# Performance work log

Hardware: AMD Instinct MI355X
Metric: run time of the kernel (lower is better)

The kernel has to match this reference:

```python
import jax, jax.numpy as jnp
import numpy as np

B, QL, KL, D, H = 2, 512, 8192, 1024, 8
HD = D // H  # head dim = 128


def setup_inputs() -> dict:
    key = jax.random.key(0)
    ks = jax.random.split(key, 12)
    s = 0.02
    return {
        "inputs_q": jax.random.normal(ks[0], (B, QL, D), jnp.float32),
        "inputs_k": jax.random.normal(ks[1], (B, KL, D), jnp.float32),
        "inputs_v": jax.random.normal(ks[2], (B, KL, D), jnp.float32),
        "attention_mask": jax.random.randint(ks[3], (B, QL, KL), 0, 2).astype(bool),
        "Wq": jax.random.normal(ks[4], (D, D), jnp.float32) * s,
        "bq": jnp.zeros((D,), jnp.float32),
        "Wk": jax.random.normal(ks[5], (D, D), jnp.float32) * s,
        "bk": jnp.zeros((D,), jnp.float32),
        "Wv": jax.random.normal(ks[6], (D, D), jnp.float32) * s,
        "bv": jnp.zeros((D,), jnp.float32),
        "Wf": jax.random.normal(ks[7], (D, D), jnp.float32) * s,
        "bf": jnp.zeros((D,), jnp.float32),
    }


def reference(inputs_q, inputs_k, inputs_v, attention_mask, Wq, bq, Wk, bk, Wv, bv, Wf, bf):
    # Projections (torch Linear: x @ W.T + b)
    q = inputs_q @ Wq.T + bq  # [B, QL, D]
    k = inputs_k @ Wk.T + bk  # [B, KL, D]
    v = inputs_v @ Wv.T + bv  # [B, KL, D]

    q = q.reshape(B, QL, H, HD)
    k = k.reshape(B, KL, H, HD)
    v = v.reshape(B, KL, H, HD)

    # scores [B, H, QL, KL]
    scores = jnp.einsum("bqhd,bkhd->bhqk", q, k)
    scale = 1.0 / np.sqrt(HD).astype(np.float32)
    scores = scores * scale
    large_k = jnp.float32(1e30)
    scores = jnp.where(attention_mask[:, None, :, :], scores, -large_k)

    probs = jax.nn.softmax(scores, axis=-1)
    # note: original calls self.dropout(normalized) but discards the result -> no-op

    summed = jnp.einsum("bhqk,bkhd->bqhd", probs, v).reshape(B, QL, H * HD)

    # wipe rows whose mask is all zero
    wipe = jnp.all(~attention_mask, axis=2, keepdims=True)  # [B, QL, 1]
    summed = jnp.where(wipe, jnp.zeros_like(summed), summed)

    return summed @ Wf.T + bf
```

## Files before the change

### kernel.cpp

```cpp
#include <hip/hip_runtime.h>
#include <hip/hip_bf16.h>
#include <math.h>

typedef __attribute__((ext_vector_type(4))) float fx4;
typedef __attribute__((ext_vector_type(4))) short sx4;
typedef __attribute__((ext_vector_type(8))) short sx8;
typedef unsigned long long u64;

#define MFMA16(a, b, c) __builtin_amdgcn_mfma_f32_16x16x16bf16_1k(a, b, c, 0, 0, 0)
#define MFMA32(a, b, c) __builtin_amdgcn_mfma_f32_16x16x32_bf16(a, b, c, 0, 0, 0)

__device__ __forceinline__ unsigned short f2bf(float f) {
  unsigned int u = __float_as_uint(f);
  return (unsigned short)((u + 0x7fffu + ((u >> 16) & 1u)) >> 16);
}

typedef const __attribute__((address_space(1))) char* gc1p;
typedef __attribute__((address_space(3))) char* lc3p;
__device__ __forceinline__ void glds16(const void* g, const void* lds_uniform) {
  gc1p gp = (gc1p)(unsigned long long)(uintptr_t)g;
  lc3p lp = (lc3p)(unsigned)__builtin_amdgcn_readfirstlane((int)(unsigned)(uintptr_t)lds_uniform);
  __builtin_amdgcn_global_load_lds(gp, lp, 16, 0, 0);
}

__global__ __launch_bounds__(256) void k_prep(
    const float* __restrict__ ink, const float* __restrict__ inv,
    const float* __restrict__ inq, const float* __restrict__ Wq,
    const float* __restrict__ Wk, const float* __restrict__ Wv,
    const float* __restrict__ Wf, const int* __restrict__ mask, short* ck,
    short* cv, short* cq, short* cwq, short* cwk, short* cwv, short* cwf,
    u64* __restrict__ mb) {
  __shared__ unsigned char nib[256];
  const int bx = blockIdx.x;
  const int t = threadIdx.x;
  if (bx >= 18944) {
    const int mbx = bx - 18944;
    const int4 m = *(const int4*)(mask + (size_t)mbx * 1024 + t * 4);
    nib[t] = (unsigned char)((m.x != 0) | ((m.y != 0) << 1) | ((m.z != 0) << 2) |
                             ((m.w != 0) << 3));
    __syncthreads();
    if (t < 16) {
      u64 wv = 0;
#pragma unroll
      for (int i = 0; i < 16; i++) wv |= (u64)(nib[t * 16 + i] & 0xF) << (4 * i);
      mb[(size_t)mbx * 16 + t] = wv;
    }
    return;
  }
  const float* s;
  short* d;
  size_t i;
  if (bx < 8192) {
    s = ink; d = ck; i = (size_t)bx * 2048;
  } else if (bx < 16384) {
    s = inv; d = cv; i = (size_t)(bx - 8192) * 2048;
  } else if (bx < 16896) {
    s = inq; d = cq; i = (size_t)(bx - 16384) * 2048;
  } else {
    const int r = bx - 16896;
    const int seg = r >> 9;
    s = seg == 0 ? Wq : seg == 1 ? Wk : seg == 2 ? Wv : Wf;
    d = seg == 0 ? cwq : seg == 1 ? cwk : seg == 2 ? cwv : cwf;
    i = (size_t)(r & 511) * 2048;
  }
  i += (size_t)t * 8;
  const fx4 a = *(const fx4*)(s + i);
  const fx4 b = *(const fx4*)(s + i + 4);
  sx8 o;
  o[0] = (short)f2bf(a[0]); o[1] = (short)f2bf(a[1]);
  o[2] = (short)f2bf(a[2]); o[3] = (short)f2bf(a[3]);
  o[4] = (short)f2bf(b[0]); o[5] = (short)f2bf(b[1]);
  o[6] = (short)f2bf(b[2]); o[7] = (short)f2bf(b[3]);
  *(sx8*)(d + i) = o;
}

template <int MODE, int MT>
__device__ __forceinline__ void gemm_body(short* sA, short* sB,
                                          const short* __restrict__ A,
                                          const short* __restrict__ Bw,
                                          const float* __restrict__ bias,
                                          void* __restrict__ Cptr, int M, int N,
                                          int K, float alpha, int bx) {
  const int t = threadIdx.x;
  const int lane = t & 63;
  const int w = t >> 6;
  const int quad = lane >> 4;
  const int l16 = lane & 15;
  const int x7 = l16 & 7;
  int m0, n0;
  if (M >= 8192) {
    const int ml = bx & 7, nn = (bx >> 3) & 7, mh = bx >> 6;
    m0 = (mh * 8 + ml) * MT;
    n0 = nn << 7;
  } else {
    const int ntile = N >> 7;
    n0 = (bx % ntile) << 7;
    m0 = (bx / ntile) * MT;
  }
  constexpr int NI = (MT == 128) ? 4 : 2;
  const int wm = (MT == 128) ? ((w >> 1) << 6) : 0;
  const int wn = (MT == 128) ? ((w & 1) << 6) : (w << 5);
  const fx4 fzero = {0.f, 0.f, 0.f, 0.f};
  fx4 acc[4][NI];
#pragma unroll
  for (int i = 0; i < 4; i++)
#pragma unroll
    for (int j = 0; j < NI; j++) acc[i][j] = fzero;

  const int srow = lane >> 3;
  const int scb = lane & 7;

  for (int k0 = 0; k0 < K; k0 += 64) {
    __syncthreads();
    if (MT == 128) {
#pragma unroll
      for (int j = 0; j < 4; j++) {
        const int row = w * 32 + j * 8 + srow;
        const int cb = scb ^ (row & 7);
        glds16(A + (size_t)(m0 + row) * K + k0 + cb * 8, &sA[(w * 32 + j * 8) * 64]);
      }
    } else {
#pragma unroll
      for (int j = 0; j < 2; j++) {
        const int row = j * 32 + w * 8 + srow;
        const int cb = scb ^ (row & 7);
        glds16(A + (size_t)(m0 + row) * K + k0 + cb * 8, &sA[(j * 32 + w * 8) * 64]);
      }
    }
#pragma unroll
    for (int j = 0; j < 4; j++) {
      const int row = w * 32 + j * 8 + srow;
      const int cb = scb ^ (row & 7);
      glds16(Bw + (size_t)(n0 + row) * K + k0 + cb * 8, &sB[(w * 32 + j * 8) * 64]);
    }
    __syncthreads();
#pragma unroll
    for (int kc = 0; kc < 2; kc++) {
      const int cbp = ((kc * 4 + quad) ^ x7) * 8;
      sx8 fa[4], fb[NI];
#pragma unroll
      for (int i = 0; i < 4; i++)
        fa[i] = *(const sx8*)(&sA[(wm + i * 16 + l16) * 64 + cbp]);
#pragma unroll
      for (int i = 0; i < NI; i++)
        fb[i] = *(const sx8*)(&sB[(wn + i * 16 + l16) * 64 + cbp]);
#pragma unroll
      for (int mi = 0; mi < 4; mi++)
#pragma unroll
        for (int ni = 0; ni < NI; ni++)
          acc[mi][ni] = MFMA32(fa[mi], fb[ni], acc[mi][ni]);
    }
  }
#pragma unroll
  for (int ni = 0; ni < NI; ni++) {
    const int col = n0 + wn + ni * 16 + l16;
    const float bval = bias[col];
    if (MODE == 2) {
#pragma unroll
      for (int mi = 0; mi < 4; mi++) {
        const int rowb = m0 + wm + mi * 16 + quad * 4;
        const int bb = rowb >> 13;
        const int kl = (rowb & 8191) ^ ((col & 8) ? 4 : 0);
        sx4 pkv;
#pragma unroll
        for (int r = 0; r < 4; r++) pkv[r] = (short)f2bf(acc[mi][ni][r] + bval);
        *(sx4*)((unsigned short*)Cptr + ((size_t)bb * 1024 + col) * 8192 + kl) = pkv;
      }
    } else {
#pragma unroll
      for (int mi = 0; mi < 4; mi++)
#pragma unroll
        for (int r = 0; r < 4; r++) {
          const int row = m0 + wm + mi * 16 + quad * 4 + r;
          const float v = (acc[mi][ni][r] + bval) * alpha;
          if (MODE == 1) ((float*)Cptr)[(size_t)row * N + col] = v;
          else ((unsigned short*)Cptr)[(size_t)row * N + col] = f2bf(v);
        }
    }
  }
}

__global__ __launch_bounds__(256) void k_gemm_k(const short* __restrict__ ck,
                                                const short* __restrict__ cwk,
                                                const float* __restrict__ bk,
                                                short* __restrict__ Kp) {
  __shared__ __align__(16) short smem[16384];
  gemm_body<0, 128>(smem, smem + 8192, ck, cwk, bk, Kp, 16384, 1024, 1024, 1.f,
                    blockIdx.x);
}

__global__ __launch_bounds__(256) void k_proj_vq(
    const short* __restrict__ cv, const short* __restrict__ cwv,
    const float* __restrict__ bv, short* __restrict__ Vt,
    const short* __restrict__ cq, const short* __restrict__ cwq,
    const float* __restrict__ bq, short* __restrict__ Qp, float alpha_q) {
  __shared__ __align__(16) short smem[16384];
  const int bx = blockIdx.x;
  if (bx < 128)
    gemm_body<0, 64>(smem, smem + 8192, cq, cwq, bq, Qp, 1024, 1024, 1024,
                     alpha_q, bx);
  else
    gemm_body<2, 128>(smem, smem + 8192, cv, cwv, bv, Vt, 16384, 1024, 1024,
                      1.f, bx - 128);
}

__global__ __launch_bounds__(256) void k_gemm_out(const short* __restrict__ summed,
                                                  const short* __restrict__ cwf,
                                                  const float* __restrict__ bf,
                                                  float* __restrict__ out) {
  __shared__ __align__(16) short smem[16384];
  gemm_body<1, 64>(smem, smem + 8192, summed, cwf, bf, out, 1024, 1024, 1024,
                   1.f, blockIdx.x);
}

__global__ __launch_bounds__(256, 4) void k_attn(const short* __restrict__ Qp,
                                                 const short* __restrict__ Kp,
                                                 const short* __restrict__ Vt,
                                                 const u64* __restrict__ mb,
                                                 float* __restrict__ ml,
                                                 float* __restrict__ Op) {
  __shared__ __align__(16) short sK[8192];
  __shared__ __align__(16) short sV[8192];
  const int x = blockIdx.x;
  const int gl = x & 7;
  const int qt = (x >> 3) & 7;
  const int gh = x >> 6;
  const int g = gh * 8 + gl;
  const int s = g & 7;
  const int h = (g >> 3) & 7;
  const int b = g >> 6;
  const int li = ((b * 8 + h) * 8 + qt) * 8 + s;
  const int t = threadIdx.x;
  const int lane = t & 63;
  const int w = t >> 6;
  const int quad = lane >> 4;
  const int l16 = lane & 15;
  const int x7 = l16 & 7;
  const int q0 = qt << 6;
  const fx4 fzero = {0.f, 0.f, 0.f, 0.f};

  const short* qbase = Qp + (size_t)(b * 512 + q0 + w * 16 + l16) * 1024 + h * 128;
  sx8 aq[4];
#pragma unroll
  for (int kc = 0; kc < 4; kc++) aq[kc] = *(const sx8*)(qbase + kc * 32 + quad * 8);

  fx4 Ot[8];
#pragma unroll
  for (int d = 0; d < 8; d++) Ot[d] = fzero;
  float lsum = 0.f;

  const short* kbase = Kp + (size_t)(b * 8192 + s * 1024) * 1024 + h * 128;
  const short* vbase = Vt + (size_t)(b * 1024 + h * 128) * 8192 + s * 1024;
  const u64* wdp = mb + (size_t)(b * 512 + q0 + w * 16 + l16) * 128 + s * 16;
  const int srow4 = lane >> 4, scb16 = lane & 15;
  const int srow8 = lane >> 3, scb8 = lane & 7;
  const int h4 = ((quad & 1) ^ ((l16 >> 3) & 1)) * 4;

  for (int kt = 0; kt < 16; kt++) {
    __syncthreads();
#pragma unroll
    for (int j = 0; j < 4; j++) {
      const int row = (w * 4 + j) * 4 + srow4;
      const int cb = scb16 ^ (row & 7);
      glds16(kbase + (size_t)(kt * 64 + row) * 1024 + cb * 8, &sK[(w * 4 + j) * 512]);
    }
#pragma unroll
    for (int j = 0; j < 4; j++) {
      const int row = (w * 4 + j) * 8 + srow8;
      const int cb = scb8 ^ (row & 7);
      glds16(vbase + (size_t)row * 8192 + kt * 64 + cb * 8, &sV[(w * 4 + j) * 512]);
    }
    const u64 wd = wdp[kt];
    __syncthreads();
    const unsigned lo = (unsigned)wd, hi = (unsigned)(wd >> 32);
    sx4 pk[4];
#pragma unroll
    for (int nt = 0; nt < 4; nt++) {
      fx4 a = fzero;
#pragma unroll
      for (int kc = 0; kc < 4; kc++) {
        const sx8 kf = *(const sx8*)(&sK[(nt * 16 + l16) * 128 + ((kc * 4 + quad) ^ x7) * 8]);
        a = MFMA32(kf, aq[kc], a);
      }
      const unsigned bits = (nt & 2) ? hi : lo;
      const int sh = (nt & 1) * 16 + quad * 4;
      float pv[4];
#pragma unroll
      for (int r = 0; r < 4; r++) {
        const float e = __builtin_amdgcn_exp2f(a[r]);
        pv[r] = ((bits >> (sh + r)) & 1u) ? e : 0.f;
        lsum += pv[r];
      }
      sx4 pko;
      ((unsigned*)&pko)[0] = __builtin_amdgcn_perm(
          __float_as_uint(pv[1]) + 0x8000u, __float_as_uint(pv[0]) + 0x8000u, 0x07060302u);
      ((unsigned*)&pko)[1] = __builtin_amdgcn_perm(
          __float_as_uint(pv[3]) + 0x8000u, __float_as_uint(pv[2]) + 0x8000u, 0x07060302u);
      pk[nt] = pko;
    }
#pragma unroll
    for (int dt = 0; dt < 8; dt++) {
      fx4 o = Ot[dt];
#pragma unroll
      for (int nt = 0; nt < 4; nt++) {
        const int cb = (2 * nt + (quad >> 1)) ^ x7;
        const sx4 vf = *(const sx4*)(&sV[(dt * 16 + l16) * 64 + cb * 8 + h4]);
        o = MFMA16(vf, pk[nt], o);
      }
      Ot[dt] = o;
    }
  }
  lsum += __shfl_xor(lsum, 16, 64);
  lsum += __shfl_xor(lsum, 32, 64);
  if (lane < 16) ml[(size_t)li * 64 + w * 16 + l16] = lsum;
  float* ob = Op + (size_t)li * 8192 + (w * 16 + l16) * 128 + quad * 4;
#pragma unroll
  for (int dt = 0; dt < 8; dt++) *(fx4*)(ob + dt * 16) = Ot[dt];
}

__global__ __launch_bounds__(256) void k_combine(const float* __restrict__ ml,
                                                 const float* __restrict__ Op,
                                                 short* __restrict__ summed) {
  const int xc = blockIdx.x;
  const int qt = xc & 7;
  const int h = (xc >> 3) & 7;
  const int b = xc >> 6;
  const int t = threadIdx.x;
  const int row = t >> 2;
  const int dg = (t & 3) * 32;
  float L = 0.f;
#pragma unroll
  for (int s = 0; s < 8; s++) L += ml[(size_t)(xc * 8 + s) * 64 + row];
  float o[32];
#pragma unroll
  for (int i = 0; i < 32; i++) o[i] = 0.f;
  if (L != 0.f) {
#pragma unroll
    for (int s = 0; s < 8; s++) {
      const float* src = Op + (size_t)(xc * 8 + s) * 8192 + row * 128 + dg;
#pragma unroll
      for (int i = 0; i < 8; i++) {
        const fx4 v = *(const fx4*)(src + i * 4);
        o[i * 4 + 0] += v[0]; o[i * 4 + 1] += v[1];
        o[i * 4 + 2] += v[2]; o[i * 4 + 3] += v[3];
      }
    }
    const float inv = 1.f / L;
#pragma unroll
    for (int i = 0; i < 32; i++) o[i] *= inv;
  }
  short* dst = summed + (size_t)(b * 512 + qt * 64 + row) * 1024 + h * 128 + dg;
#pragma unroll
  for (int i = 0; i < 4; i++) {
    sx8 pkv;
#pragma unroll
    for (int j = 0; j < 8; j++) pkv[j] = (short)f2bf(o[i * 8 + j]);
    *(sx8*)(dst + i * 8) = pkv;
  }
}

extern "C" void kernel_launch(void* const* d_in, const int* in_sizes, int n_in,
                              void* d_out, int out_size, void* d_ws, size_t ws_size,
                              hipStream_t stream) {
  (void)in_sizes; (void)n_in; (void)out_size; (void)ws_size;
  const float* inq = (const float*)d_in[0];
  const float* ink = (const float*)d_in[1];
  const float* inv = (const float*)d_in[2];
  const int* mask = (const int*)d_in[3];
  const float* Wq = (const float*)d_in[4];
  const float* bq = (const float*)d_in[5];
  const float* Wk = (const float*)d_in[6];
  const float* bk = (const float*)d_in[7];
  const float* Wv = (const float*)d_in[8];
  const float* bv = (const float*)d_in[9];
  const float* Wf = (const float*)d_in[10];
  const float* bf = (const float*)d_in[11];

  char* ws = (char*)d_ws;
  short* S1 = (short*)(ws + 0);
  short* Kp = (short*)(ws + 33554432);
  short* S3 = (short*)(ws + 67108864);
  short* cq = (short*)(ws + 100663296);
  short* cwq = (short*)(ws + 102760448);
  short* cwk = (short*)(ws + 104857600);
  short* cwv = (short*)(ws + 106954752);
  short* cwf = (short*)(ws + 109051904);
  short* Qp = (short*)(ws + 111149056);
  short* summed = (short*)(ws + 113246208);
  u64* mb = (u64*)(ws + 115343360);
  float* ml = (float*)(ws + 116391936);

  const float alpha_q = 0.12751757f;

  k_prep<<<27136, 256, 0, stream>>>(ink, inv, inq, Wq, Wk, Wv, Wf, mask, S1, S3,
                                    cq, cwq, cwk, cwv, cwf, mb);
  k_gemm_k<<<1024, 256, 0, stream>>>(S1, cwk, bk, Kp);
  k_proj_vq<<<1152, 256, 0, stream>>>(S3, cwv, bv, S1, cq, cwq, bq, Qp, alpha_q);
  k_attn<<<1024, 256, 0, stream>>>(Qp, Kp, S1, mb, ml, (float*)S3);
  k_combine<<<128, 256, 0, stream>>>(ml, (const float*)S3, summed);
  k_gemm_out<<<128, 256, 0, stream>>>(summed, cwf, bf, (float*)d_out);
}
```

Baseline: 388.7 us.

## Fuse fp32-to-bf16 activation conversion into projection GEMM tile loads

Removes the separate conversion pass over the Q, K and V activations in the prep kernel. The projection GEMMs now read fp32 inputs directly into registers, pack them to bf16 with v_cvt_pk_bf16_f32, and store them into the swizzled LDS tile. This drops a full write and re-read of the large bf16 copies of K and V. In exchange, the A operand no longer uses async global-to-LDS loads, so global load latency is exposed before each tile sync and register pressure rises.

```diff
diff --git a/kernel.cpp b/kernel.cpp
--- a/kernel.cpp
+++ b/kernel.cpp
@@ -13,6 +13,12 @@
 __device__ __forceinline__ unsigned short f2bf(float f) {
   unsigned int u = __float_as_uint(f);
   return (unsigned short)((u + 0x7fffu + ((u >> 16) & 1u)) >> 16);
+}
+
+__device__ __forceinline__ unsigned cvtpk(float lo, float hi) {
+  unsigned r;
+  asm("v_cvt_pk_bf16_f32 %0, %1, %2" : "=v"(r) : "v"(lo), "v"(hi));
+  return r;
 }
 
 typedef const __attribute__((address_space(1))) char* gc1p;
@@ -24,17 +30,15 @@
 }
 
 __global__ __launch_bounds__(256) void k_prep(
-    const float* __restrict__ ink, const float* __restrict__ inv,
-    const float* __restrict__ inq, const float* __restrict__ Wq,
-    const float* __restrict__ Wk, const float* __restrict__ Wv,
-    const float* __restrict__ Wf, const int* __restrict__ mask, short* ck,
-    short* cv, short* cq, short* cwq, short* cwk, short* cwv, short* cwf,
-    u64* __restrict__ mb) {
+    const float* __restrict__ Wq, const float* __restrict__ Wk,
+    const float* __restrict__ Wv, const float* __restrict__ Wf,
+    const int* __restrict__ mask, short* cwq, short* cwk, short* cwv,
+    short* cwf, u64* __restrict__ mb) {
   __shared__ unsigned char nib[256];
   const int bx = blockIdx.x;
   const int t = threadIdx.x;
-  if (bx >= 18944) {
-    const int mbx = bx - 18944;
+  if (bx >= 2048) {
+    const int mbx = bx - 2048;
     const int4 m = *(const int4*)(mask + (size_t)mbx * 1024 + t * 4);
     nib[t] = (unsigned char)((m.x != 0) | ((m.y != 0) << 1) | ((m.z != 0) << 2) |
                              ((m.w != 0) << 3));
@@ -47,23 +51,10 @@
     }
     return;
   }
-  const float* s;
-  short* d;
-  size_t i;
-  if (bx < 8192) {
-    s = ink; d = ck; i = (size_t)bx * 2048;
-  } else if (bx < 16384) {
-    s = inv; d = cv; i = (size_t)(bx - 8192) * 2048;
-  } else if (bx < 16896) {
-    s = inq; d = cq; i = (size_t)(bx - 16384) * 2048;
-  } else {
-    const int r = bx - 16896;
-    const int seg = r >> 9;
-    s = seg == 0 ? Wq : seg == 1 ? Wk : seg == 2 ? Wv : Wf;
-    d = seg == 0 ? cwq : seg == 1 ? cwk : seg == 2 ? cwv : cwf;
-    i = (size_t)(r & 511) * 2048;
-  }
-  i += (size_t)t * 8;
+  const int seg = bx >> 9;
+  const float* s = seg == 0 ? Wq : seg == 1 ? Wk : seg == 2 ? Wv : Wf;
+  short* d = seg == 0 ? cwq : seg == 1 ? cwk : seg == 2 ? cwv : cwf;
+  size_t i = (size_t)(bx & 511) * 2048 + (size_t)t * 8;
   const fx4 a = *(const fx4*)(s + i);
   const fx4 b = *(const fx4*)(s + i + 4);
   sx8 o;
@@ -74,9 +65,9 @@
   *(sx8*)(d + i) = o;
 }
 
-template <int MODE, int MT>
+template <int MODE, int MT, int AF32>
 __device__ __forceinline__ void gemm_body(short* sA, short* sB,
-                                          const short* __restrict__ A,
+                                          const void* __restrict__ Aptr,
                                           const short* __restrict__ Bw,
                                           const float* __restrict__ bias,
                                           void* __restrict__ Cptr, int M, int N,
@@ -98,6 +89,7 @@
     m0 = (bx / ntile) * MT;
   }
   constexpr int NI = (MT == 128) ? 4 : 2;
+  constexpr int NJ = (MT == 128) ? 4 : 2;
   const int wm = (MT == 128) ? ((w >> 1) << 6) : 0;
   const int wn = (MT == 128) ? ((w & 1) << 6) : (w << 5);
   const fx4 fzero = {0.f, 0.f, 0.f, 0.f};
@@ -111,20 +103,28 @@
   const int scb = lane & 7;
 
   for (int k0 = 0; k0 < K; k0 += 64) {
+    fx4 ra[NJ][2];
+    if (AF32) {
+      const float* Af = (const float*)Aptr;
+#pragma unroll
+      for (int j = 0; j < NJ; j++) {
+        const int rbase = (MT == 128) ? (w * 32 + j * 8) : (j * 32 + w * 8);
+        const int row = rbase + srow;
+        const int cb = scb ^ (row & 7);
+        const float* src = Af + (size_t)(m0 + row) * K + k0 + cb * 8;
+        ra[j][0] = *(const fx4*)src;
+        ra[j][1] = *(const fx4*)(src + 4);
+      }
+    }
     __syncthreads();
-    if (MT == 128) {
-#pragma unroll
-      for (int j = 0; j < 4; j++) {
-        const int row = w * 32 + j * 8 + srow;
+    if (!AF32) {
+      const short* A = (const short*)Aptr;
+#pragma unroll
+      for (int j = 0; j < NJ; j++) {
+        const int rbase = (MT == 128) ? (w * 32 + j * 8) : (j * 32 + w * 8);
+        const int row = rbase + srow;
         const int cb = scb ^ (row & 7);
-        glds16(A + (size_t)(m0 + row) * K + k0 + cb * 8, &sA[(w * 32 + j * 8) * 64]);
-      }
-    } else {
-#pragma unroll
-      for (int j = 0; j < 2; j++) {
-        const int row = j * 32 + w * 8 + srow;
-        const int cb = scb ^ (row & 7);
-        glds16(A + (size_t)(m0 + row) * K + k0 + cb * 8, &sA[(j * 32 + w * 8) * 64]);
+        glds16(A + (size_t)(m0 + row) * K + k0 + cb * 8, &sA[rbase * 64]);
       }
     }
 #pragma unroll
@@ -132,6 +132,19 @@
       const int row = w * 32 + j * 8 + srow;
       const int cb = scb ^ (row & 7);
       glds16(Bw + (size_t)(n0 + row) * K + k0 + cb * 8, &sB[(w * 32 + j * 8) * 64]);
+    }
+    if (AF32) {
+#pragma unroll
+      for (int j = 0; j < NJ; j++) {
+        const int rbase = (MT == 128) ? (w * 32 + j * 8) : (j * 32 + w * 8);
+        sx8 o;
+        unsigned* ou = (unsigned*)&o;
+        ou[0] = cvtpk(ra[j][0][0], ra[j][0][1]);
+        ou[1] = cvtpk(ra[j][0][2], ra[j][0][3]);
+        ou[2] = cvtpk(ra[j][1][0], ra[j][1][1]);
+        ou[3] = cvtpk(ra[j][1][2], ra[j][1][3]);
+        *(sx8*)(&sA[rbase * 64 + lane * 8]) = o;
+      }
     }
     __syncthreads();
 #pragma unroll
@@ -180,28 +193,28 @@
   }
 }
 
-__global__ __launch_bounds__(256) void k_gemm_k(const short* __restrict__ ck,
+__global__ __launch_bounds__(256) void k_gemm_k(const float* __restrict__ ink,
                                                 const short* __restrict__ cwk,
                                                 const float* __restrict__ bk,
                                                 short* __restrict__ Kp) {
   __shared__ __align__(16) short smem[16384];
-  gemm_body<0, 128>(smem, smem + 8192, ck, cwk, bk, Kp, 16384, 1024, 1024, 1.f,
-                    blockIdx.x);
+  gemm_body<0, 128, 1>(smem, smem + 8192, ink, cwk, bk, Kp, 16384, 1024, 1024,
+                       1.f, blockIdx.x);
 }
 
 __global__ __launch_bounds__(256) void k_proj_vq(
-    const short* __restrict__ cv, const short* __restrict__ cwv,
+    const float* __restrict__ inv, const short* __restrict__ cwv,
     const float* __restrict__ bv, short* __restrict__ Vt,
-    const short* __restrict__ cq, const short* __restrict__ cwq,
+    const float* __restrict__ inq, const short* __restrict__ cwq,
     const float* __restrict__ bq, short* __restrict__ Qp, float alpha_q) {
   __shared__ __align__(16) short smem[16384];
   const int bx = blockIdx.x;
   if (bx < 128)
-    gemm_body<0, 64>(smem, smem + 8192, cq, cwq, bq, Qp, 1024, 1024, 1024,
-                     alpha_q, bx);
+    gemm_body<0, 64, 1>(smem, smem + 8192, inq, cwq, bq, Qp, 1024, 1024, 1024,
+                        alpha_q, bx);
   else
-    gemm_body<2, 128>(smem, smem + 8192, cv, cwv, bv, Vt, 16384, 1024, 1024,
-                      1.f, bx - 128);
+    gemm_body<2, 128, 1>(smem, smem + 8192, inv, cwv, bv, Vt, 16384, 1024, 1024,
+                         1.f, bx - 128);
 }
 
 __global__ __launch_bounds__(256) void k_gemm_out(const short* __restrict__ summed,
@@ -209,8 +222,8 @@
                                                   const float* __restrict__ bf,
                                                   float* __restrict__ out) {
   __shared__ __align__(16) short smem[16384];
-  gemm_body<1, 64>(smem, smem + 8192, summed, cwf, bf, out, 1024, 1024, 1024,
-                   1.f, blockIdx.x);
+  gemm_body<1, 64, 0>(smem, smem + 8192, summed, cwf, bf, out, 1024, 1024, 1024,
+                      1.f, blockIdx.x);
 }
 
 __global__ __launch_bounds__(256, 4) void k_attn(const short* __restrict__ Qp,
@@ -377,10 +390,9 @@
   const float* bf = (const float*)d_in[11];
 
   char* ws = (char*)d_ws;
-  short* S1 = (short*)(ws + 0);
+  short* Vt = (short*)(ws + 0);
   short* Kp = (short*)(ws + 33554432);
-  short* S3 = (short*)(ws + 67108864);
-  short* cq = (short*)(ws + 100663296);
+  float* Op = (float*)(ws + 67108864);
   short* cwq = (short*)(ws + 102760448);
   short* cwk = (short*)(ws + 104857600);
   short* cwv = (short*)(ws + 106954752);
@@ -392,11 +404,10 @@
 
   const float alpha_q = 0.12751757f;
 
-  k_prep<<<27136, 256, 0, stream>>>(ink, inv, inq, Wq, Wk, Wv, Wf, mask, S1, S3,
-                                    cq, cwq, cwk, cwv, cwf, mb);
-  k_gemm_k<<<1024, 256, 0, stream>>>(S1, cwk, bk, Kp);
-  k_proj_vq<<<1152, 256, 0, stream>>>(S3, cwv, bv, S1, cq, cwq, bq, Qp, alpha_q);
-  k_attn<<<1024, 256, 0, stream>>>(Qp, Kp, S1, mb, ml, (float*)S3);
-  k_combine<<<128, 256, 0, stream>>>(ml, (const float*)S3, summed);
+  k_prep<<<10240, 256, 0, stream>>>(Wq, Wk, Wv, Wf, mask, cwq, cwk, cwv, cwf, mb);
+  k_gemm_k<<<1024, 256, 0, stream>>>(ink, cwk, bk, Kp);
+  k_proj_vq<<<1152, 256, 0, stream>>>(inv, cwv, bv, Vt, inq, cwq, bq, Qp, alpha_q);
+  k_attn<<<1024, 256, 0, stream>>>(Qp, Kp, Vt, mb, ml, Op);
+  k_combine<<<128, 256, 0, stream>>>(ml, Op, summed);
   k_gemm_out<<<128, 256, 0, stream>>>(summed, cwf, bf, (float*)d_out);
 }
```

Measured after the change: 405.2 us. 4.3% more time.
